# Kernel optimization log

Measured on AMD Instinct MI355X. Metric: run time of the kernel, lower is better.

Reference implementation:

```python
import jax, jax.numpy as jnp
import numpy as np

N_WORD, N_TOPIC, N_DOC = 50000, 2000, 50000
D_WORD, D_TOPIC, D_OUT = 256, 128, 128
E_WW, E_WT, E_WD, E_TD, E_TT = 500000, 400000, 500000, 400000, 300000


def setup_inputs() -> dict:
    key = jax.random.key(0)
    ks = jax.random.split(key, 32)
    i = iter(range(32))

    def randn(shape, scale=1.0):
        return jax.random.normal(ks[next(i)], shape, dtype=jnp.float32) * scale

    def edges(n_e, n_src, n_dst):
        src = jax.random.randint(ks[next(i)], (n_e,), 0, n_src, dtype=jnp.int32)
        dst = jax.random.randint(ks[next(i)], (n_e,), 0, n_dst, dtype=jnp.int32)
        w = jax.random.uniform(ks[next(i)], (n_e,), dtype=jnp.float32)
        return src, dst, w

    feat_word = randn((N_WORD, D_WORD))
    feat_topic = randn((N_TOPIC, D_TOPIC))
    ww_src, ww_dst, ww_w = edges(E_WW, N_WORD, N_WORD)
    wt_src, wt_dst, wt_w = edges(E_WT, N_WORD, N_TOPIC)
    wd_src, wd_dst, wd_w = edges(E_WD, N_WORD, N_DOC)
    td_src, td_dst, td_w = edges(E_TD, N_TOPIC, N_DOC)
    tt_src, tt_dst, tt_w = edges(E_TT, N_TOPIC, N_TOPIC)
    return dict(
        feat_word=feat_word, feat_topic=feat_topic,
        ww_src=ww_src, ww_dst=ww_dst, ww_w=ww_w,
        wt_src=wt_src, wt_dst=wt_dst, wt_w=wt_w,
        wd_src=wd_src, wd_dst=wd_dst, wd_w=wd_w,
        td_src=td_src, td_dst=td_dst, td_w=td_w,
        tt_src=tt_src, tt_dst=tt_dst, tt_w=tt_w,
        W_ww=randn((D_WORD, D_OUT), 0.02), b_ww=randn((D_OUT,), 0.02),
        W_wt=randn((D_WORD, D_OUT), 0.02), b_wt=randn((D_OUT,), 0.02),
        W_wd=randn((D_WORD, D_OUT), 0.02), b_wd=randn((D_OUT,), 0.02),
        W_td=randn((D_TOPIC, D_OUT), 0.02), b_td=randn((D_OUT,), 0.02),
        W_tt=randn((D_TOPIC, D_OUT), 0.02), b_tt=randn((D_OUT,), 0.02),
    )


def _mean_agg(Wh, src, dst, w, n_dst):
    # u_mul_e: gather src feature, scale by edge weight; fn.mean: divide by in-degree
    m = Wh[src] * w[:, None]                                   # [E, D_OUT]
    s = jax.ops.segment_sum(m, dst, num_segments=n_dst)        # [n_dst, D_OUT]
    deg = jax.ops.segment_sum(jnp.ones_like(w), dst, num_segments=n_dst)
    return jnp.where(deg[:, None] > 0, s / jnp.maximum(deg, 1.0)[:, None], 0.0)


def reference(feat_word, feat_topic,
              ww_src, ww_dst, ww_w, wt_src, wt_dst, wt_w,
              wd_src, wd_dst, wd_w, td_src, td_dst, td_w,
              tt_src, tt_dst, tt_w,
              W_ww, b_ww, W_wt, b_wt, W_wd, b_wd, W_td, b_td, W_tt, b_tt):
    # Per-relation projections (note: in the torch source the causal/noise
    # branches are overwritten by the plain Linear, so this is the effective math).
    Wh_ww = feat_word @ W_ww + b_ww
    Wh_wt = feat_word @ W_wt + b_wt
    Wh_wd = feat_word @ W_wd + b_wd
    Wh_td = feat_topic @ W_td + b_td
    Wh_tt = feat_topic @ W_tt + b_tt
    # mean per edge type, then cross-etype 'sum' per destination node type
    h_word = _mean_agg(Wh_ww, ww_src, ww_dst, ww_w, N_WORD)
    h_topic = (_mean_agg(Wh_wt, wt_src, wt_dst, wt_w, N_TOPIC)
               + _mean_agg(Wh_tt, tt_src, tt_dst, tt_w, N_TOPIC))
    h_doc = (_mean_agg(Wh_wd, wd_src, wd_dst, wd_w, N_DOC)
             + _mean_agg(Wh_td, td_src, td_dst, td_w, N_DOC))
    return h_word, h_topic, h_doc
```

## Files before the change

kernel.cpp:

```cpp
#include <hip/hip_runtime.h>

typedef short short8 __attribute__((ext_vector_type(8)));
typedef float floatx4 __attribute__((ext_vector_type(4)));

__device__ __forceinline__ float b2f(unsigned int u16) {
    union { unsigned int i; float f; } v;
    v.i = u16 << 16;
    return v.f;
}
__device__ __forceinline__ unsigned short f2b(float f) {
    unsigned int i = __float_as_uint(f);
    unsigned int r = (i + 0x7FFFu + ((i >> 16) & 1u)) >> 16;
    return (unsigned short)r;
}

#define N_WORD  50000
#define N_TOPIC 2000
#define N_DOC   50000
#define E_MAX   500000
#define CHAIN_END 0xFFFFFFFFu
#define NB_GEMM 814

__global__ void detect_kernel(const unsigned int* __restrict__ feat_u32,
                              unsigned int* __restrict__ flag)
{
    int cnt = 0;
    for (int i = 0; i < 256; ++i) {
        unsigned int u = feat_u32[i];
        int e = (u >> 7) & 0xFF;
        if (e >= 110 && e <= 140) ++cnt;
    }
    *flag = (cnt > 128) ? 1u : 0u;
}

__global__ __launch_bounds__(256) void swizzle_kernel(
    const void* __restrict__ W0, const void* __restrict__ W1,
    const void* __restrict__ W2, const void* __restrict__ W3,
    const void* __restrict__ W4,
    const void* __restrict__ b0, const void* __restrict__ b1,
    const void* __restrict__ b2, const void* __restrict__ b3,
    const void* __restrict__ b4,
    short8* __restrict__ D0, short8* __restrict__ D1,
    short8* __restrict__ D2, short8* __restrict__ D3,
    short8* __restrict__ D4,
    unsigned short* __restrict__ bias_out,
    const unsigned int* __restrict__ flag_p)
{
    const int w = blockIdx.y;
    const void* W; const void* bs; short8* D; int S;
    switch (w) {
        case 0: W = W0; bs = b0; D = D0; S = 8; break;
        case 1: W = W1; bs = b1; D = D1; S = 8; break;
        case 2: W = W2; bs = b2; D = D2; S = 8; break;
        case 3: W = W3; bs = b3; D = D3; S = 4; break;
        default: W = W4; bs = b4; D = D4; S = 4; break;
    }
    const int n_entries = S * 8 * 64;
    const int mode = (int)*flag_p;
    for (int e = blockIdx.x * 256 + threadIdx.x; e < n_entries; e += 8 * 256) {
        const int lane = e & 63, t = (e >> 6) & 7, s = e >> 9;
        const int q = lane >> 4, n = t * 16 + (lane & 15);
        short8 val;
#pragma unroll
        for (int j = 0; j < 8; ++j) {
            const int k = s * 32 + q * 8 + j;
            unsigned short hv = mode ? ((const unsigned short*)W)[k * 128 + n]
                                     : f2b(((const float*)W)[k * 128 + n]);
            val[j] = (short)hv;
        }
        D[e] = val;
    }
    if (blockIdx.x == 0 && threadIdx.x < 128) {
        bias_out[w * 128 + threadIdx.x] =
            mode ? ((const unsigned short*)bs)[threadIdx.x]
                 : f2b(((const float*)bs)[threadIdx.x]);
    }
}

template <int S, int NP>
__device__ __forceinline__ void gemm_body_lds(
    short8* __restrict__ Blds,
    const void* feat_, int n_rows, int bx,
    const short8* Ba, const short8* Bb, const short8* Bc,
    const unsigned short* bias_all, int ba, int bb, int bc,
    unsigned short* Oa, unsigned short* Ob, unsigned short* Oc,
    int mode_bf16)
{
    const int tid = threadIdx.x;
    const int lane = tid & 63;
    const int wave = tid >> 6;
    const int row0 = (bx * 4 + wave) * 16;
    const int m = lane & 15, q = lane >> 4;
    const int K = S * 32;
    int arow_idx = row0 + m;
    if (arow_idx >= n_rows) arow_idx = n_rows - 1;

    short8 a[S];
    if (mode_bf16) {
        const short8* arow = (const short8*)((const unsigned short*)feat_ + (size_t)arow_idx * K);
#pragma unroll
        for (int s = 0; s < S; ++s) a[s] = arow[s * 4 + q];
    } else {
        const float* arow = (const float*)feat_ + (size_t)arow_idx * K;
#pragma unroll
        for (int s = 0; s < S; ++s) {
            const float4 f0 = ((const float4*)arow)[s * 8 + q * 2];
            const float4 f1 = ((const float4*)arow)[s * 8 + q * 2 + 1];
            short8 t;
            t[0] = (short)f2b(f0.x); t[1] = (short)f2b(f0.y);
            t[2] = (short)f2b(f0.z); t[3] = (short)f2b(f0.w);
            t[4] = (short)f2b(f1.x); t[5] = (short)f2b(f1.y);
            t[6] = (short)f2b(f1.z); t[7] = (short)f2b(f1.w);
            a[s] = t;
        }
    }

    constexpr int NH = (S * 8 * 64 > 2048) ? 2 : 1;
    constexpr int SH = S / NH;

#pragma unroll
    for (int p = 0; p < NP; ++p) {
        const short8* B = (p == 0) ? Ba : ((p == 1) ? Bb : Bc);
        const unsigned short* bias = bias_all + ((p == 0) ? ba : ((p == 1) ? bb : bc)) * 128;
        unsigned short* O = (p == 0) ? Oa : ((p == 1) ? Ob : Oc);

        floatx4 acc[8];
#pragma unroll
        for (int t = 0; t < 8; ++t) { acc[t][0] = 0.f; acc[t][1] = 0.f; acc[t][2] = 0.f; acc[t][3] = 0.f; }

#pragma unroll
        for (int h = 0; h < NH; ++h) {
            __syncthreads();
            for (int i = tid; i < SH * 8 * 64; i += 256) Blds[i] = B[h * (SH * 8 * 64) + i];
            __syncthreads();
#pragma unroll
            for (int s = 0; s < SH; ++s) {
#pragma unroll
                for (int t = 0; t < 8; ++t) {
                    short8 b = Blds[(s * 8 + t) * 64 + lane];
                    acc[t] = __builtin_amdgcn_mfma_f32_16x16x32_bf16(a[h * SH + s], b, acc[t], 0, 0, 0);
                }
            }
        }

#pragma unroll
        for (int t = 0; t < 8; ++t) {
            const float bb_ = b2f((unsigned int)bias[t * 16 + m]);
#pragma unroll
            for (int r = 0; r < 4; ++r) {
                const int row = row0 + q * 4 + r;
                if (row < n_rows)
                    O[(size_t)row * 128 + t * 16 + m] = f2b(acc[t][r] + bb_);
            }
        }
    }
}

__global__ __launch_bounds__(256) void link_gemm_kernel(
    const void* __restrict__ feat_word, const void* __restrict__ feat_topic,
    const short8* __restrict__ Bww, const short8* __restrict__ Bwt,
    const short8* __restrict__ Bwd, const short8* __restrict__ Btt,
    const short8* __restrict__ Btd,
    const unsigned short* __restrict__ bias_all,
    unsigned short* __restrict__ Wh_ww, unsigned short* __restrict__ Wh_wt,
    unsigned short* __restrict__ Wh_wd, unsigned short* __restrict__ Wh_tt,
    unsigned short* __restrict__ Wh_td,
    const int* s0, const int* d0, const void* w0, int n0, unsigned int* h0, unsigned long long* e0,
    const int* s1, const int* d1, const void* w1, int n1, unsigned int* h1, unsigned long long* e1,
    const int* s2, const int* d2, const void* w2, int n2, unsigned int* h2, unsigned long long* e2,
    const int* s3, const int* d3, const void* w3, int n3, unsigned int* h3, unsigned long long* e3,
    const int* s4, const int* d4, const void* w4, int n4, unsigned int* h4, unsigned long long* e4,
    const unsigned int* __restrict__ flag_p)
{
    __shared__ short8 Blds[2048];
    const int mode = (int)*flag_p;

    if (blockIdx.x < NB_GEMM) {
        if (blockIdx.x < 782) {
            gemm_body_lds<8, 3>(Blds, feat_word, N_WORD, blockIdx.x, Bww, Bwt, Bwd,
                                bias_all, 0, 1, 2, Wh_ww, Wh_wt, Wh_wd, mode);
        } else {
            gemm_body_lds<4, 2>(Blds, feat_topic, N_TOPIC, blockIdx.x - 782, Btt, Btd,
                                (const short8*)nullptr, bias_all, 4, 3, 0,
                                Wh_tt, Wh_td, (unsigned short*)nullptr, mode);
        }
        return;
    }

    int lb = blockIdx.x - NB_GEMM;
    const int nb0 = (n0 + 255) >> 8, nb1 = (n1 + 255) >> 8, nb2 = (n2 + 255) >> 8,
              nb3 = (n3 + 255) >> 8;
    const int* src; const int* dst; const void* w_; int n;
    unsigned int* head; unsigned long long* ent; int H;
    if (lb < nb0)      { src = s0; dst = d0; w_ = w0; n = n0; head = h0; ent = e0; H = 1; }
    else if ((lb -= nb0) < nb1) { src = s1; dst = d1; w_ = w1; n = n1; head = h1; ent = e1; H = 4; }
    else if ((lb -= nb1) < nb2) { src = s2; dst = d2; w_ = w2; n = n2; head = h2; ent = e2; H = 4; }
    else if ((lb -= nb2) < nb3) { src = s3; dst = d3; w_ = w3; n = n3; head = h3; ent = e3; H = 1; }
    else { lb -= nb3;  src = s4; dst = d4; w_ = w4; n = n4; head = h4; ent = e4; H = 1; }

    const int i = lb * 256 + threadIdx.x;
    if (i >= n) return;
    const int d = dst[i];
    const unsigned int slot = (unsigned int)d * H + ((unsigned int)i & (H - 1));
    const unsigned int old = atomicExch(&head[slot], (unsigned int)i);
    const unsigned short w16 = mode ? ((const unsigned short*)w_)[i]
                                    : f2b(((const float*)w_)[i]);
    ent[i] = ((unsigned long long)old << 32)
           | ((unsigned long long)w16 << 16)
           | (unsigned long long)(unsigned int)src[i];
}

__device__ __forceinline__ void chain8(
    const unsigned long long* __restrict__ ent,
    const unsigned short* __restrict__ Wh,
    unsigned int e, int sl, float a[8], float& cnt)
{
    while (e != CHAIN_END) {
        const unsigned long long v = ent[e];
        const unsigned int lo = (unsigned int)v;
        e = (unsigned int)(v >> 32);
        const float w = b2f(lo >> 16);
        const uint4 u = ((const uint4*)(Wh + (size_t)(lo & 0xffffu) * 128))[sl];
        a[0] += b2f(u.x & 0xffffu) * w; a[1] += b2f(u.x >> 16) * w;
        a[2] += b2f(u.y & 0xffffu) * w; a[3] += b2f(u.y >> 16) * w;
        a[4] += b2f(u.z & 0xffffu) * w; a[5] += b2f(u.z >> 16) * w;
        a[6] += b2f(u.w & 0xffffu) * w; a[7] += b2f(u.w >> 16) * w;
        cnt += 1.0f;
    }
}

__device__ __forceinline__ void write8(
    void* out, size_t off_elems, int node, int sl, const float r[8], int mode)
{
    if (mode) {
        uint4 o;
        o.x = (unsigned int)f2b(r[0]) | ((unsigned int)f2b(r[1]) << 16);
        o.y = (unsigned int)f2b(r[2]) | ((unsigned int)f2b(r[3]) << 16);
        o.z = (unsigned int)f2b(r[4]) | ((unsigned int)f2b(r[5]) << 16);
        o.w = (unsigned int)f2b(r[6]) | ((unsigned int)f2b(r[7]) << 16);
        *(uint4*)((unsigned short*)out + off_elems + (size_t)node * 128 + sl * 8) = o;
    } else {
        float* p = (float*)out + off_elems + (size_t)node * 128 + sl * 8;
        ((float4*)p)[0] = make_float4(r[0], r[1], r[2], r[3]);
        ((float4*)p)[1] = make_float4(r[4], r[5], r[6], r[7]);
    }
}

__global__ __launch_bounds__(256) void gather_dt_kernel(
    const unsigned int* __restrict__ h_wt, const unsigned long long* __restrict__ e_wt,
    const unsigned short* __restrict__ Wh_wt,
    const unsigned int* __restrict__ h_tt, const unsigned long long* __restrict__ e_tt,
    const unsigned short* __restrict__ Wh_tt,
    const unsigned int* __restrict__ h_wd, const unsigned long long* __restrict__ e_wd,
    const unsigned short* __restrict__ Wh_wd,
    const unsigned int* __restrict__ h_td, const unsigned long long* __restrict__ e_td,
    const unsigned short* __restrict__ Wh_td,
    void* __restrict__ out,
    const unsigned int* __restrict__ flag_p)
{
    const int mode = (int)*flag_p;
    const int sl = threadIdx.x & 15;

    if (blockIdx.x < 500) {
        const int wave = threadIdx.x >> 6;
        const int grp  = (threadIdx.x >> 4) & 3;
        const int node = blockIdx.x * 4 + wave;
        float r[8] = {0, 0, 0, 0, 0, 0, 0, 0};
        {
            float a[8] = {0, 0, 0, 0, 0, 0, 0, 0}; float cnt = 0.f;
            chain8(e_wt, Wh_wt, h_wt[node * 4 + grp], sl, a, cnt);
#pragma unroll
            for (int j = 0; j < 8; ++j) { a[j] += __shfl_xor(a[j], 16); a[j] += __shfl_xor(a[j], 32); }
            cnt += __shfl_xor(cnt, 16); cnt += __shfl_xor(cnt, 32);
            const float inv = (cnt > 0.f) ? 1.f / cnt : 0.f;
#pragma unroll
            for (int j = 0; j < 8; ++j) r[j] += a[j] * inv;
        }
        {
            float a[8] = {0, 0, 0, 0, 0, 0, 0, 0}; float cnt = 0.f;
            chain8(e_tt, Wh_tt, h_tt[node * 4 + grp], sl, a, cnt);
#pragma unroll
            for (int j = 0; j < 8; ++j) { a[j] += __shfl_xor(a[j], 16); a[j] += __shfl_xor(a[j], 32); }
            cnt += __shfl_xor(cnt, 16); cnt += __shfl_xor(cnt, 32);
            const float inv = (cnt > 0.f) ? 1.f / cnt : 0.f;
#pragma unroll
            for (int j = 0; j < 8; ++j) r[j] += a[j] * inv;
        }
        if (grp == 0) write8(out, (size_t)6400000, node, sl, r, mode);
    } else {
        const int sub = threadIdx.x >> 4;
        const int node = (blockIdx.x - 500) * 16 + sub;
        float r[8] = {0, 0, 0, 0, 0, 0, 0, 0};
        {
            float a[8] = {0, 0, 0, 0, 0, 0, 0, 0}; float cnt = 0.f;
            chain8(e_wd, Wh_wd, h_wd[node], sl, a, cnt);
            const float inv = (cnt > 0.f) ? 1.f / cnt : 0.f;
#pragma unroll
            for (int j = 0; j < 8; ++j) r[j] += a[j] * inv;
        }
        {
            float a[8] = {0, 0, 0, 0, 0, 0, 0, 0}; float cnt = 0.f;
            chain8(e_td, Wh_td, h_td[node], sl, a, cnt);
            const float inv = (cnt > 0.f) ? 1.f / cnt : 0.f;
#pragma unroll
            for (int j = 0; j < 8; ++j) r[j] += a[j] * inv;
        }
        write8(out, (size_t)6656000, node, sl, r, mode);
    }
}

__global__ __launch_bounds__(256) void gather_w_kernel(
    const unsigned int* __restrict__ h_ww, const unsigned long long* __restrict__ e_ww,
    const unsigned short* __restrict__ Wh_ww,
    void* __restrict__ out,
    const unsigned int* __restrict__ flag_p)
{
    const int mode = (int)*flag_p;
    const int sl = threadIdx.x & 15;
    const int sub = threadIdx.x >> 4;
    const int node = blockIdx.x * 16 + sub;
    float a[8] = {0, 0, 0, 0, 0, 0, 0, 0}; float cnt = 0.f;
    chain8(e_ww, Wh_ww, h_ww[node], sl, a, cnt);
    const float inv = (cnt > 0.f) ? 1.f / cnt : 0.f;
#pragma unroll
    for (int j = 0; j < 8; ++j) a[j] *= inv;
    write8(out, 0, node, sl, a, mode);
}

extern "C" void kernel_launch(void* const* d_in, const int* in_sizes, int n_in,
                              void* d_out, int out_size, void* d_ws, size_t ws_size,
                              hipStream_t stream)
{
    const void* feat_word  = d_in[0];
    const void* feat_topic = d_in[1];
    const int* ww_src = (const int*)d_in[2];
    const int* ww_dst = (const int*)d_in[3];
    const void* ww_w = d_in[4];
    const int* wt_src = (const int*)d_in[5];
    const int* wt_dst = (const int*)d_in[6];
    const void* wt_w = d_in[7];
    const int* wd_src = (const int*)d_in[8];
    const int* wd_dst = (const int*)d_in[9];
    const void* wd_w = d_in[10];
    const int* td_src = (const int*)d_in[11];
    const int* td_dst = (const int*)d_in[12];
    const void* td_w = d_in[13];
    const int* tt_src = (const int*)d_in[14];
    const int* tt_dst = (const int*)d_in[15];
    const void* tt_w = d_in[16];
    const void* W_ww = d_in[17];
    const void* b_ww = d_in[18];
    const void* W_wt = d_in[19];
    const void* b_wt = d_in[20];
    const void* W_wd = d_in[21];
    const void* b_wd = d_in[22];
    const void* W_td = d_in[23];
    const void* b_td = d_in[24];
    const void* W_tt = d_in[25];
    const void* b_tt = d_in[26];

    const int E_ww = in_sizes[2];
    const int E_wt = in_sizes[5];
    const int E_wd = in_sizes[8];
    const int E_td = in_sizes[11];
    const int E_tt = in_sizes[14];

    char* ws = (char*)d_ws;
    unsigned int* flag = (unsigned int*)ws;
    unsigned int* head_base = (unsigned int*)(ws + 4);
    unsigned int* h_ww = head_base;
    unsigned int* h_wt = h_ww + 50000;
    unsigned int* h_tt = h_wt + 8000;
    unsigned int* h_wd = h_tt + 8000;
    unsigned int* h_td = h_wd + 50000;
    size_t off = 4 + (size_t)166000 * 4;
    off = (off + 15) & ~(size_t)15;
    short8* Bsw_ww = (short8*)(ws + off); off += 65536;
    short8* Bsw_wt = (short8*)(ws + off); off += 65536;
    short8* Bsw_wd = (short8*)(ws + off); off += 65536;
    short8* Bsw_td = (short8*)(ws + off); off += 32768;
    short8* Bsw_tt = (short8*)(ws + off); off += 32768;
    unsigned short* bias_all = (unsigned short*)(ws + off); off += 5 * 128 * 2;
    off = (off + 15) & ~(size_t)15;
    unsigned short* Wh_ww = (unsigned short*)(ws + off); off += (size_t)N_WORD * 128 * 2;
    unsigned short* Wh_wt = (unsigned short*)(ws + off); off += (size_t)N_WORD * 128 * 2;
    unsigned short* Wh_tt = (unsigned short*)(ws + off); off += (size_t)N_TOPIC * 128 * 2;
    unsigned short* Wh_td = (unsigned short*)(ws + off); off += (size_t)N_TOPIC * 128 * 2;
    off = (off + 7) & ~(size_t)7;
    unsigned long long* e_ww = (unsigned long long*)(ws + off); off += (size_t)E_MAX * 8;
    unsigned long long* e_wt = (unsigned long long*)(ws + off); off += (size_t)E_MAX * 8;
    unsigned long long* e_tt = (unsigned long long*)(ws + off); off += (size_t)E_MAX * 8;
    unsigned long long* e_wd = (unsigned long long*)(ws + off); off += (size_t)E_MAX * 8;
    unsigned long long* e_td = (unsigned long long*)(ws + off); off += (size_t)E_MAX * 8;

    unsigned short* Wh_wd = (unsigned short*)d_out;

    detect_kernel<<<1, 1, 0, stream>>>((const unsigned int*)feat_word, flag);
    hipMemsetAsync(head_base, 0xFF, (size_t)166000 * 4, stream);

    swizzle_kernel<<<dim3(8, 5), 256, 0, stream>>>(
        W_ww, W_wt, W_wd, W_td, W_tt, b_ww, b_wt, b_wd, b_td, b_tt,
        Bsw_ww, Bsw_wt, Bsw_wd, Bsw_td, Bsw_tt, bias_all, flag);

    const int nb_link = ((E_ww + 255) / 256) + ((E_wt + 255) / 256) +
                        ((E_tt + 255) / 256) + ((E_wd + 255) / 256) +
                        ((E_td + 255) / 256);
    link_gemm_kernel<<<NB_GEMM + nb_link, 256, 0, stream>>>(
        feat_word, feat_topic, Bsw_ww, Bsw_wt, Bsw_wd, Bsw_tt, Bsw_td,
        bias_all, Wh_ww, Wh_wt, Wh_wd, Wh_tt, Wh_td,
        ww_src, ww_dst, ww_w, E_ww, h_ww, e_ww,
        wt_src, wt_dst, wt_w, E_wt, h_wt, e_wt,
        tt_src, tt_dst, tt_w, E_tt, h_tt, e_tt,
        wd_src, wd_dst, wd_w, E_wd, h_wd, e_wd,
        td_src, td_dst, td_w, E_td, h_td, e_td, flag);

    gather_dt_kernel<<<500 + 3125, 256, 0, stream>>>(
        h_wt, e_wt, Wh_wt, h_tt, e_tt, Wh_tt,
        h_wd, e_wd, Wh_wd, h_td, e_td, Wh_td, d_out, flag);

    gather_w_kernel<<<3125, 256, 0, stream>>>(
        h_ww, e_ww, Wh_ww, d_out, flag);
}
```

Measured before the change: 402.4 us.

## Interleave GEMM and link blocks, batch edge linking, fuse gather kernels

Link blocks now process four edges per thread, and GEMM blocks are interleaved with link blocks (2 of every 7) so the two kinds of work overlap on the device instead of running in sequence. When the workspace is large enough, Wh_wd moves from the output buffer into the workspace. That removes the ordering hazard with the word gather, so the topic, doc and word gathers run in a single fused kernel launch instead of two. The cost is extra workspace and more index arithmetic, and the added atomics per thread may raise contention.

```diff
diff --git a/kernel.cpp b/kernel.cpp
--- a/kernel.cpp
+++ b/kernel.cpp
@@ -174,22 +174,29 @@
 {
     __shared__ short8 Blds[2048];
     const int mode = (int)*flag_p;
-
-    if (blockIdx.x < NB_GEMM) {
-        if (blockIdx.x < 782) {
-            gemm_body_lds<8, 3>(Blds, feat_word, N_WORD, blockIdx.x, Bww, Bwt, Bwd,
-                                bias_all, 0, 1, 2, Wh_ww, Wh_wt, Wh_wd, mode);
-        } else {
-            gemm_body_lds<4, 2>(Blds, feat_topic, N_TOPIC, blockIdx.x - 782, Btt, Btd,
-                                (const short8*)nullptr, bias_all, 4, 3, 0,
-                                Wh_tt, Wh_td, (unsigned short*)nullptr, mode);
+    const int bid = blockIdx.x;
+    const int q7 = bid / 7, r7 = bid % 7;
+
+    if (r7 < 2) {
+        const int gid = q7 * 2 + r7;
+        if (gid < NB_GEMM) {
+            if (gid < 782) {
+                gemm_body_lds<8, 3>(Blds, feat_word, N_WORD, gid, Bww, Bwt, Bwd,
+                                    bias_all, 0, 1, 2, Wh_ww, Wh_wt, Wh_wd, mode);
+            } else {
+                gemm_body_lds<4, 2>(Blds, feat_topic, N_TOPIC, gid - 782, Btt, Btd,
+                                    (const short8*)nullptr, bias_all, 4, 3, 0,
+                                    Wh_tt, Wh_td, (unsigned short*)nullptr, mode);
+            }
+            return;
         }
-        return;
-    }
-
-    int lb = blockIdx.x - NB_GEMM;
-    const int nb0 = (n0 + 255) >> 8, nb1 = (n1 + 255) >> 8, nb2 = (n2 + 255) >> 8,
-              nb3 = (n3 + 255) >> 8;
+    }
+
+    const int cnt_g = min(q7 * 2 + min(r7, 2), NB_GEMM);
+    int lb = bid - cnt_g;
+
+    const int nb0 = (n0 + 1023) >> 10, nb1 = (n1 + 1023) >> 10,
+              nb2 = (n2 + 1023) >> 10, nb3 = (n3 + 1023) >> 10;
     const int* src; const int* dst; const void* w_; int n;
     unsigned int* head; unsigned long long* ent; int H;
     if (lb < nb0)      { src = s0; dst = d0; w_ = w0; n = n0; head = h0; ent = e0; H = 1; }
@@ -198,16 +205,27 @@
     else if ((lb -= nb2) < nb3) { src = s3; dst = d3; w_ = w3; n = n3; head = h3; ent = e3; H = 1; }
     else { lb -= nb3;  src = s4; dst = d4; w_ = w4; n = n4; head = h4; ent = e4; H = 1; }
 
-    const int i = lb * 256 + threadIdx.x;
-    if (i >= n) return;
-    const int d = dst[i];
-    const unsigned int slot = (unsigned int)d * H + ((unsigned int)i & (H - 1));
-    const unsigned int old = atomicExch(&head[slot], (unsigned int)i);
-    const unsigned short w16 = mode ? ((const unsigned short*)w_)[i]
-                                    : f2b(((const float*)w_)[i]);
-    ent[i] = ((unsigned long long)old << 32)
-           | ((unsigned long long)w16 << 16)
-           | (unsigned long long)(unsigned int)src[i];
+    const int i0 = lb * 1024 + threadIdx.x;
+    bool val[4]; int iv[4]; unsigned long long lo[4]; unsigned int oldv[4];
+#pragma unroll
+    for (int u = 0; u < 4; ++u) {
+        const int i = i0 + u * 256;
+        iv[u] = i;
+        val[u] = (i < n);
+        if (val[u]) {
+            const int d = dst[i];
+            const unsigned short w16 = mode ? ((const unsigned short*)w_)[i]
+                                            : f2b(((const float*)w_)[i]);
+            lo[u] = ((unsigned long long)w16 << 16)
+                  | (unsigned long long)(unsigned int)src[i];
+            const unsigned int slot = (unsigned int)d * H + ((unsigned int)i & (H - 1));
+            oldv[u] = atomicExch(&head[slot], (unsigned int)i);
+        }
+    }
+#pragma unroll
+    for (int u = 0; u < 4; ++u)
+        if (val[u])
+            ent[iv[u]] = ((unsigned long long)oldv[u] << 32) | lo[u];
 }
 
 __device__ __forceinline__ void chain8(
@@ -246,6 +264,110 @@
     }
 }
 
+__device__ __forceinline__ void topic_body(
+    const unsigned int* __restrict__ h_wt, const unsigned long long* __restrict__ e_wt,
+    const unsigned short* __restrict__ Wh_wt,
+    const unsigned int* __restrict__ h_tt, const unsigned long long* __restrict__ e_tt,
+    const unsigned short* __restrict__ Wh_tt,
+    void* __restrict__ out, int blk, int mode)
+{
+    const int sl = threadIdx.x & 15;
+    const int wave = threadIdx.x >> 6;
+    const int grp  = (threadIdx.x >> 4) & 3;
+    const int node = blk * 4 + wave;
+    float r[8] = {0, 0, 0, 0, 0, 0, 0, 0};
+    {
+        float a[8] = {0, 0, 0, 0, 0, 0, 0, 0}; float cnt = 0.f;
+        chain8(e_wt, Wh_wt, h_wt[node * 4 + grp], sl, a, cnt);
+#pragma unroll
+        for (int j = 0; j < 8; ++j) { a[j] += __shfl_xor(a[j], 16); a[j] += __shfl_xor(a[j], 32); }
+        cnt += __shfl_xor(cnt, 16); cnt += __shfl_xor(cnt, 32);
+        const float inv = (cnt > 0.f) ? 1.f / cnt : 0.f;
+#pragma unroll
+        for (int j = 0; j < 8; ++j) r[j] += a[j] * inv;
+    }
+    {
+        float a[8] = {0, 0, 0, 0, 0, 0, 0, 0}; float cnt = 0.f;
+        chain8(e_tt, Wh_tt, h_tt[node * 4 + grp], sl, a, cnt);
+#pragma unroll
+        for (int j = 0; j < 8; ++j) { a[j] += __shfl_xor(a[j], 16); a[j] += __shfl_xor(a[j], 32); }
+        cnt += __shfl_xor(cnt, 16); cnt += __shfl_xor(cnt, 32);
+        const float inv = (cnt > 0.f) ? 1.f / cnt : 0.f;
+#pragma unroll
+        for (int j = 0; j < 8; ++j) r[j] += a[j] * inv;
+    }
+    if (grp == 0) write8(out, (size_t)6400000, node, sl, r, mode);
+}
+
+__device__ __forceinline__ void doc_body(
+    const unsigned int* __restrict__ h_a, const unsigned long long* __restrict__ e_a,
+    const unsigned short* __restrict__ Wh_a,
+    const unsigned int* __restrict__ h_b, const unsigned long long* __restrict__ e_b,
+    const unsigned short* __restrict__ Wh_b,
+    void* __restrict__ out, size_t off_elems, int blk, int mode)
+{
+    const int sl = threadIdx.x & 15;
+    const int sub = threadIdx.x >> 4;
+    const int node = blk * 16 + sub;
+    float r[8] = {0, 0, 0, 0, 0, 0, 0, 0};
+    {
+        float a[8] = {0, 0, 0, 0, 0, 0, 0, 0}; float cnt = 0.f;
+        chain8(e_a, Wh_a, h_a[node], sl, a, cnt);
+        const float inv = (cnt > 0.f) ? 1.f / cnt : 0.f;
+#pragma unroll
+        for (int j = 0; j < 8; ++j) r[j] += a[j] * inv;
+    }
+    {
+        float a[8] = {0, 0, 0, 0, 0, 0, 0, 0}; float cnt = 0.f;
+        chain8(e_b, Wh_b, h_b[node], sl, a, cnt);
+        const float inv = (cnt > 0.f) ? 1.f / cnt : 0.f;
+#pragma unroll
+        for (int j = 0; j < 8; ++j) r[j] += a[j] * inv;
+    }
+    write8(out, off_elems, node, sl, r, mode);
+}
+
+__device__ __forceinline__ void word_body(
+    const unsigned int* __restrict__ h_ww, const unsigned long long* __restrict__ e_ww,
+    const unsigned short* __restrict__ Wh_ww,
+    void* __restrict__ out, int blk, int mode)
+{
+    const int sl = threadIdx.x & 15;
+    const int sub = threadIdx.x >> 4;
+    const int node = blk * 16 + sub;
+    float a[8] = {0, 0, 0, 0, 0, 0, 0, 0}; float cnt = 0.f;
+    chain8(e_ww, Wh_ww, h_ww[node], sl, a, cnt);
+    const float inv = (cnt > 0.f) ? 1.f / cnt : 0.f;
+#pragma unroll
+    for (int j = 0; j < 8; ++j) a[j] *= inv;
+    write8(out, 0, node, sl, a, mode);
+}
+
+__global__ __launch_bounds__(256) void gather_all_kernel(
+    const unsigned int* __restrict__ h_wt, const unsigned long long* __restrict__ e_wt,
+    const unsigned short* __restrict__ Wh_wt,
+    const unsigned int* __restrict__ h_tt, const unsigned long long* __restrict__ e_tt,
+    const unsigned short* __restrict__ Wh_tt,
+    const unsigned int* __restrict__ h_wd, const unsigned long long* __restrict__ e_wd,
+    const unsigned short* __restrict__ Wh_wd,
+    const unsigned int* __restrict__ h_td, const unsigned long long* __restrict__ e_td,
+    const unsigned short* __restrict__ Wh_td,
+    const unsigned int* __restrict__ h_ww, const unsigned long long* __restrict__ e_ww,
+    const unsigned short* __restrict__ Wh_ww,
+    void* __restrict__ out,
+    const unsigned int* __restrict__ flag_p)
+{
+    const int mode = (int)*flag_p;
+    if (blockIdx.x < 500) {
+        topic_body(h_wt, e_wt, Wh_wt, h_tt, e_tt, Wh_tt, out, blockIdx.x, mode);
+    } else if (blockIdx.x < 3625) {
+        doc_body(h_wd, e_wd, Wh_wd, h_td, e_td, Wh_td,
+                 out, (size_t)6656000, blockIdx.x - 500, mode);
+    } else {
+        word_body(h_ww, e_ww, Wh_ww, out, blockIdx.x - 3625, mode);
+    }
+}
+
 __global__ __launch_bounds__(256) void gather_dt_kernel(
     const unsigned int* __restrict__ h_wt, const unsigned long long* __restrict__ e_wt,
     const unsigned short* __restrict__ Wh_wt,
@@ -259,53 +381,11 @@
     const unsigned int* __restrict__ flag_p)
 {
     const int mode = (int)*flag_p;
-    const int sl = threadIdx.x & 15;
-
     if (blockIdx.x < 500) {
-        const int wave = threadIdx.x >> 6;
-        const int grp  = (threadIdx.x >> 4) & 3;
-        const int node = blockIdx.x * 4 + wave;
-        float r[8] = {0, 0, 0, 0, 0, 0, 0, 0};
-        {
-            float a[8] = {0, 0, 0, 0, 0, 0, 0, 0}; float cnt = 0.f;
-            chain8(e_wt, Wh_wt, h_wt[node * 4 + grp], sl, a, cnt);
-#pragma unroll
-            for (int j = 0; j < 8; ++j) { a[j] += __shfl_xor(a[j], 16); a[j] += __shfl_xor(a[j], 32); }
-            cnt += __shfl_xor(cnt, 16); cnt += __shfl_xor(cnt, 32);
-            const float inv = (cnt > 0.f) ? 1.f / cnt : 0.f;
-#pragma unroll
-            for (int j = 0; j < 8; ++j) r[j] += a[j] * inv;
-        }
-        {
-            float a[8] = {0, 0, 0, 0, 0, 0, 0, 0}; float cnt = 0.f;
-            chain8(e_tt, Wh_tt, h_tt[node * 4 + grp], sl, a, cnt);
-#pragma unroll
-            for (int j = 0; j < 8; ++j) { a[j] += __shfl_xor(a[j], 16); a[j] += __shfl_xor(a[j], 32); }
-            cnt += __shfl_xor(cnt, 16); cnt += __shfl_xor(cnt, 32);
-            const float inv = (cnt > 0.f) ? 1.f / cnt : 0.f;
-#pragma unroll
-            for (int j = 0; j < 8; ++j) r[j] += a[j] * inv;
-        }
-        if (grp == 0) write8(out, (size_t)6400000, node, sl, r, mode);
+        topic_body(h_wt, e_wt, Wh_wt, h_tt, e_tt, Wh_tt, out, blockIdx.x, mode);
     } else {
-        const int sub = threadIdx.x >> 4;
-        const int node = (blockIdx.x - 500) * 16 + sub;
-        float r[8] = {0, 0, 0, 0, 0, 0, 0, 0};
-        {
-            float a[8] = {0, 0, 0, 0, 0, 0, 0, 0}; float cnt = 0.f;
-            chain8(e_wd, Wh_wd, h_wd[node], sl, a, cnt);
-            const float inv = (cnt > 0.f) ? 1.f / cnt : 0.f;
-#pragma unroll
-            for (int j = 0; j < 8; ++j) r[j] += a[j] * inv;
-        }
-        {
-            float a[8] = {0, 0, 0, 0, 0, 0, 0, 0}; float cnt = 0.f;
-            chain8(e_td, Wh_td, h_td[node], sl, a, cnt);
-            const float inv = (cnt > 0.f) ? 1.f / cnt : 0.f;
-#pragma unroll
-            for (int j = 0; j < 8; ++j) r[j] += a[j] * inv;
-        }
-        write8(out, (size_t)6656000, node, sl, r, mode);
+        doc_body(h_wd, e_wd, Wh_wd, h_td, e_td, Wh_td,
+                 out, (size_t)6656000, blockIdx.x - 500, mode);
     }
 }
 
@@ -315,16 +395,7 @@
     void* __restrict__ out,
     const unsigned int* __restrict__ flag_p)
 {
-    const int mode = (int)*flag_p;
-    const int sl = threadIdx.x & 15;
-    const int sub = threadIdx.x >> 4;
-    const int node = blockIdx.x * 16 + sub;
-    float a[8] = {0, 0, 0, 0, 0, 0, 0, 0}; float cnt = 0.f;
-    chain8(e_ww, Wh_ww, h_ww[node], sl, a, cnt);
-    const float inv = (cnt > 0.f) ? 1.f / cnt : 0.f;
-#pragma unroll
-    for (int j = 0; j < 8; ++j) a[j] *= inv;
-    write8(out, 0, node, sl, a, mode);
+    word_body(h_ww, e_ww, Wh_ww, out, blockIdx.x, (int)*flag_p);
 }
 
 extern "C" void kernel_launch(void* const* d_in, const int* in_sizes, int n_in,
@@ -393,7 +464,11 @@
     unsigned long long* e_wd = (unsigned long long*)(ws + off); off += (size_t)E_MAX * 8;
     unsigned long long* e_td = (unsigned long long*)(ws + off); off += (size_t)E_MAX * 8;
 
-    unsigned short* Wh_wd = (unsigned short*)d_out;
+    off = (off + 15) & ~(size_t)15;
+    const size_t whwd_bytes = (size_t)N_WORD * 128 * 2;
+    const bool fuse_gather = (ws_size >= off + whwd_bytes);
+    unsigned short* Wh_wd = fuse_gather ? (unsigned short*)(ws + off)
+                                        : (unsigned short*)d_out;
 
     detect_kernel<<<1, 1, 0, stream>>>((const unsigned int*)feat_word, flag);
     hipMemsetAsync(head_base, 0xFF, (size_t)166000 * 4, stream);
@@ -402,10 +477,12 @@
         W_ww, W_wt, W_wd, W_td, W_tt, b_ww, b_wt, b_wd, b_td, b_tt,
         Bsw_ww, Bsw_wt, Bsw_wd, Bsw_td, Bsw_tt, bias_all, flag);
 
-    const int nb_link = ((E_ww + 255) / 256) + ((E_wt + 255) / 256) +
-                        ((E_tt + 255) / 256) + ((E_wd + 255) / 256) +
-                        ((E_td + 255) / 256);
-    link_gemm_kernel<<<NB_GEMM + nb_link, 256, 0, stream>>>(
+    const int nb_link = ((E_ww + 1023) / 1024) + ((E_wt + 1023) / 1024) +
+                        ((E_tt + 1023) / 1024) + ((E_wd + 1023) / 1024) +
+                        ((E_td + 1023) / 1024);
+    int n_blocks = NB_GEMM + nb_link;
+    if (n_blocks < 2844) n_blocks = 2844;
+    link_gemm_kernel<<<n_blocks, 256, 0, stream>>>(
         feat_word, feat_topic, Bsw_ww, Bsw_wt, Bsw_wd, Bsw_tt, Bsw_td,
         bias_all, Wh_ww, Wh_wt, Wh_wd, Wh_tt, Wh_td,
         ww_src, ww_dst, ww_w, E_ww, h_ww, e_ww,
@@ -414,10 +491,16 @@
         wd_src, wd_dst, wd_w, E_wd, h_wd, e_wd,
         td_src, td_dst, td_w, E_td, h_td, e_td, flag);
 
-    gather_dt_kernel<<<500 + 3125, 256, 0, stream>>>(
-        h_wt, e_wt, Wh_wt, h_tt, e_tt, Wh_tt,
-        h_wd, e_wd, Wh_wd, h_td, e_td, Wh_td, d_out, flag);
-
-    gather_w_kernel<<<3125, 256, 0, stream>>>(
-        h_ww, e_ww, Wh_ww, d_out, flag);
-}
+    if (fuse_gather) {
+        gather_all_kernel<<<500 + 3125 + 3125, 256, 0, stream>>>(
+            h_wt, e_wt, Wh_wt, h_tt, e_tt, Wh_tt,
+            h_wd, e_wd, Wh_wd, h_td, e_td, Wh_td,
+            h_ww, e_ww, Wh_ww, d_out, flag);
+    } else {
+        gather_dt_kernel<<<500 + 3125, 256, 0, stream>>>(
+            h_wt, e_wt, Wh_wt, h_tt, e_tt, Wh_tt,
+            h_wd, e_wd, Wh_wd, h_td, e_td, Wh_td, d_out, flag);
+        gather_w_kernel<<<3125, 256, 0, stream>>>(
+            h_ww, e_ww, Wh_ww, d_out, flag);
+    }
+}
```

Measured after the change: 401.6 us. Within noise of the previous version (-0.2%).

## Split all edge chains four ways, prefetch chain links, and fuse gathers into one kernel

Applied to the files above, without the earlier changes.

Every relation's linked-list head now uses four sub-chains per destination node. Each node is handled by a full wave that reduces the sub-chains with shuffles, which shortens serial pointer-chasing depth. The chain walk prefetches the next entry while gathering the current row, and walks two relations at once to overlap their latencies. When workspace allows, Wh_wd is moved out of the output buffer so all three gathers fuse into one launch. In exchange, head-array memset size grows and the gather launches use four times as many blocks, with more shuffle-reduction work.

```diff
diff --git a/kernel.cpp b/kernel.cpp
--- a/kernel.cpp
+++ b/kernel.cpp
@@ -20,6 +20,12 @@
 #define E_MAX   500000
 #define CHAIN_END 0xFFFFFFFFu
 #define NB_GEMM 814
+#define NSLOT_WW 200000
+#define NSLOT_WT 8000
+#define NSLOT_TT 8000
+#define NSLOT_WD 200000
+#define NSLOT_TD 200000
+#define NSLOT_ALL (NSLOT_WW + NSLOT_WT + NSLOT_TT + NSLOT_WD + NSLOT_TD)
 
 __global__ void detect_kernel(const unsigned int* __restrict__ feat_u32,
                               unsigned int* __restrict__ flag)
@@ -191,17 +197,17 @@
     const int nb0 = (n0 + 255) >> 8, nb1 = (n1 + 255) >> 8, nb2 = (n2 + 255) >> 8,
               nb3 = (n3 + 255) >> 8;
     const int* src; const int* dst; const void* w_; int n;
-    unsigned int* head; unsigned long long* ent; int H;
-    if (lb < nb0)      { src = s0; dst = d0; w_ = w0; n = n0; head = h0; ent = e0; H = 1; }
-    else if ((lb -= nb0) < nb1) { src = s1; dst = d1; w_ = w1; n = n1; head = h1; ent = e1; H = 4; }
-    else if ((lb -= nb1) < nb2) { src = s2; dst = d2; w_ = w2; n = n2; head = h2; ent = e2; H = 4; }
-    else if ((lb -= nb2) < nb3) { src = s3; dst = d3; w_ = w3; n = n3; head = h3; ent = e3; H = 1; }
-    else { lb -= nb3;  src = s4; dst = d4; w_ = w4; n = n4; head = h4; ent = e4; H = 1; }
+    unsigned int* head; unsigned long long* ent;
+    if (lb < nb0)      { src = s0; dst = d0; w_ = w0; n = n0; head = h0; ent = e0; }
+    else if ((lb -= nb0) < nb1) { src = s1; dst = d1; w_ = w1; n = n1; head = h1; ent = e1; }
+    else if ((lb -= nb1) < nb2) { src = s2; dst = d2; w_ = w2; n = n2; head = h2; ent = e2; }
+    else if ((lb -= nb2) < nb3) { src = s3; dst = d3; w_ = w3; n = n3; head = h3; ent = e3; }
+    else { lb -= nb3;  src = s4; dst = d4; w_ = w4; n = n4; head = h4; ent = e4; }
 
     const int i = lb * 256 + threadIdx.x;
     if (i >= n) return;
     const int d = dst[i];
-    const unsigned int slot = (unsigned int)d * H + ((unsigned int)i & (H - 1));
+    const unsigned int slot = (unsigned int)d * 4 + ((unsigned int)i & 3);
     const unsigned int old = atomicExch(&head[slot], (unsigned int)i);
     const unsigned short w16 = mode ? ((const unsigned short*)w_)[i]
                                     : f2b(((const float*)w_)[i]);
@@ -210,22 +216,52 @@
            | (unsigned long long)(unsigned int)src[i];
 }
 
-__device__ __forceinline__ void chain8(
+__device__ __forceinline__ void acc8(float a[8], const uint4& u, float w)
+{
+    a[0] += b2f(u.x & 0xffffu) * w; a[1] += b2f(u.x >> 16) * w;
+    a[2] += b2f(u.y & 0xffffu) * w; a[3] += b2f(u.y >> 16) * w;
+    a[4] += b2f(u.z & 0xffffu) * w; a[5] += b2f(u.z >> 16) * w;
+    a[6] += b2f(u.w & 0xffffu) * w; a[7] += b2f(u.w >> 16) * w;
+}
+
+__device__ __forceinline__ void walk1(
     const unsigned long long* __restrict__ ent,
     const unsigned short* __restrict__ Wh,
     unsigned int e, int sl, float a[8], float& cnt)
 {
-    while (e != CHAIN_END) {
-        const unsigned long long v = ent[e];
-        const unsigned int lo = (unsigned int)v;
-        e = (unsigned int)(v >> 32);
-        const float w = b2f(lo >> 16);
-        const uint4 u = ((const uint4*)(Wh + (size_t)(lo & 0xffffu) * 128))[sl];
-        a[0] += b2f(u.x & 0xffffu) * w; a[1] += b2f(u.x >> 16) * w;
-        a[2] += b2f(u.y & 0xffffu) * w; a[3] += b2f(u.y >> 16) * w;
-        a[4] += b2f(u.z & 0xffffu) * w; a[5] += b2f(u.z >> 16) * w;
-        a[6] += b2f(u.w & 0xffffu) * w; a[7] += b2f(u.w >> 16) * w;
+    bool live = (e != CHAIN_END);
+    unsigned long long v = ent[live ? e : 0];
+    while (live) {
+        const unsigned int nx = (unsigned int)(v >> 32);
+        const bool live_n = (nx != CHAIN_END);
+        const unsigned long long vn = ent[live_n ? nx : 0];
+        const uint4 u = ((const uint4*)(Wh + (size_t)((unsigned int)v & 0xffffu) * 128))[sl];
+        acc8(a, u, b2f(((unsigned int)v) >> 16));
         cnt += 1.0f;
+        v = vn; live = live_n;
+    }
+}
+
+__device__ __forceinline__ void walk2(
+    const unsigned long long* __restrict__ ent1, const unsigned short* __restrict__ Wh1, unsigned int e1,
+    const unsigned long long* __restrict__ ent2, const unsigned short* __restrict__ Wh2, unsigned int e2,
+    int sl, float a1[8], float a2[8], float& c1, float& c2)
+{
+    bool l1 = (e1 != CHAIN_END), l2 = (e2 != CHAIN_END);
+    unsigned long long v1 = ent1[l1 ? e1 : 0];
+    unsigned long long v2 = ent2[l2 ? e2 : 0];
+    while (l1 || l2) {
+        const unsigned int n1 = (unsigned int)(v1 >> 32);
+        const unsigned int n2 = (unsigned int)(v2 >> 32);
+        const bool l1n = l1 && (n1 != CHAIN_END);
+        const bool l2n = l2 && (n2 != CHAIN_END);
+        const unsigned long long v1n = ent1[l1n ? n1 : 0];
+        const unsigned long long v2n = ent2[l2n ? n2 : 0];
+        const uint4 u1 = ((const uint4*)(Wh1 + (size_t)((unsigned int)v1 & 0xffffu) * 128))[sl];
+        const uint4 u2 = ((const uint4*)(Wh2 + (size_t)((unsigned int)v2 & 0xffffu) * 128))[sl];
+        if (l1) { acc8(a1, u1, b2f(((unsigned int)v1) >> 16)); c1 += 1.0f; }
+        if (l2) { acc8(a2, u2, b2f(((unsigned int)v2) >> 16)); c2 += 1.0f; }
+        v1 = v1n; v2 = v2n; l1 = l1n; l2 = l2n;
     }
 }
 
@@ -246,6 +282,83 @@
     }
 }
 
+__device__ __forceinline__ void dual_body(
+    const unsigned int* __restrict__ h1, const unsigned long long* __restrict__ e1t,
+    const unsigned short* __restrict__ Wh1,
+    const unsigned int* __restrict__ h2, const unsigned long long* __restrict__ e2t,
+    const unsigned short* __restrict__ Wh2,
+    void* __restrict__ out, size_t off_elems, int blk, int mode)
+{
+    const int sl = threadIdx.x & 15;
+    const int grp = (threadIdx.x >> 4) & 3;
+    const int wave = threadIdx.x >> 6;
+    const int node = blk * 4 + wave;
+    float a1[8] = {0,0,0,0,0,0,0,0}, a2[8] = {0,0,0,0,0,0,0,0};
+    float c1 = 0.f, c2 = 0.f;
+    walk2(e1t, Wh1, h1[node * 4 + grp], e2t, Wh2, h2[node * 4 + grp],
+          sl, a1, a2, c1, c2);
+#pragma unroll
+    for (int j = 0; j < 8; ++j) {
+        a1[j] += __shfl_xor(a1[j], 16); a1[j] += __shfl_xor(a1[j], 32);
+        a2[j] += __shfl_xor(a2[j], 16); a2[j] += __shfl_xor(a2[j], 32);
+    }
+    c1 += __shfl_xor(c1, 16); c1 += __shfl_xor(c1, 32);
+    c2 += __shfl_xor(c2, 16); c2 += __shfl_xor(c2, 32);
+    const float i1 = (c1 > 0.f) ? 1.f / c1 : 0.f;
+    const float i2 = (c2 > 0.f) ? 1.f / c2 : 0.f;
+    float r[8];
+#pragma unroll
+    for (int j = 0; j < 8; ++j) r[j] = a1[j] * i1 + a2[j] * i2;
+    if (grp == 0) write8(out, off_elems, node, sl, r, mode);
+}
+
+__device__ __forceinline__ void word_body(
+    const unsigned int* __restrict__ h_ww, const unsigned long long* __restrict__ e_ww,
+    const unsigned short* __restrict__ Wh_ww,
+    void* __restrict__ out, int blk, int mode)
+{
+    const int sl = threadIdx.x & 15;
+    const int grp = (threadIdx.x >> 4) & 3;
+    const int wave = threadIdx.x >> 6;
+    const int node = blk * 4 + wave;
+    float a[8] = {0,0,0,0,0,0,0,0}; float cnt = 0.f;
+    walk1(e_ww, Wh_ww, h_ww[node * 4 + grp], sl, a, cnt);
+#pragma unroll
+    for (int j = 0; j < 8; ++j) { a[j] += __shfl_xor(a[j], 16); a[j] += __shfl_xor(a[j], 32); }
+    cnt += __shfl_xor(cnt, 16); cnt += __shfl_xor(cnt, 32);
+    const float inv = (cnt > 0.f) ? 1.f / cnt : 0.f;
+    float r[8];
+#pragma unroll
+    for (int j = 0; j < 8; ++j) r[j] = a[j] * inv;
+    if (grp == 0) write8(out, 0, node, sl, r, mode);
+}
+
+__global__ __launch_bounds__(256) void gather_all_kernel(
+    const unsigned int* __restrict__ h_wt, const unsigned long long* __restrict__ e_wt,
+    const unsigned short* __restrict__ Wh_wt,
+    const unsigned int* __restrict__ h_tt, const unsigned long long* __restrict__ e_tt,
+    const unsigned short* __restrict__ Wh_tt,
+    const unsigned int* __restrict__ h_wd, const unsigned long long* __restrict__ e_wd,
+    const unsigned short* __restrict__ Wh_wd,
+    const unsigned int* __restrict__ h_td, const unsigned long long* __restrict__ e_td,
+    const unsigned short* __restrict__ Wh_td,
+    const unsigned int* __restrict__ h_ww, const unsigned long long* __restrict__ e_ww,
+    const unsigned short* __restrict__ Wh_ww,
+    void* __restrict__ out,
+    const unsigned int* __restrict__ flag_p)
+{
+    const int mode = (int)*flag_p;
+    if (blockIdx.x < 500) {
+        dual_body(h_wt, e_wt, Wh_wt, h_tt, e_tt, Wh_tt,
+                  out, (size_t)6400000, blockIdx.x, mode);
+    } else if (blockIdx.x < 13000) {
+        dual_body(h_wd, e_wd, Wh_wd, h_td, e_td, Wh_td,
+                  out, (size_t)6656000, blockIdx.x - 500, mode);
+    } else {
+        word_body(h_ww, e_ww, Wh_ww, out, blockIdx.x - 13000, mode);
+    }
+}
+
 __global__ __launch_bounds__(256) void gather_dt_kernel(
     const unsigned int* __restrict__ h_wt, const unsigned long long* __restrict__ e_wt,
     const unsigned short* __restrict__ Wh_wt,
@@ -259,53 +372,12 @@
     const unsigned int* __restrict__ flag_p)
 {
     const int mode = (int)*flag_p;
-    const int sl = threadIdx.x & 15;
-
     if (blockIdx.x < 500) {
-        const int wave = threadIdx.x >> 6;
-        const int grp  = (threadIdx.x >> 4) & 3;
-        const int node = blockIdx.x * 4 + wave;
-        float r[8] = {0, 0, 0, 0, 0, 0, 0, 0};
-        {
-            float a[8] = {0, 0, 0, 0, 0, 0, 0, 0}; float cnt = 0.f;
-            chain8(e_wt, Wh_wt, h_wt[node * 4 + grp], sl, a, cnt);
-#pragma unroll
-            for (int j = 0; j < 8; ++j) { a[j] += __shfl_xor(a[j], 16); a[j] += __shfl_xor(a[j], 32); }
-            cnt += __shfl_xor(cnt, 16); cnt += __shfl_xor(cnt, 32);
-            const float inv = (cnt > 0.f) ? 1.f / cnt : 0.f;
-#pragma unroll
-            for (int j = 0; j < 8; ++j) r[j] += a[j] * inv;
-        }
-        {
-            float a[8] = {0, 0, 0, 0, 0, 0, 0, 0}; float cnt = 0.f;
-            chain8(e_tt, Wh_tt, h_tt[node * 4 + grp], sl, a, cnt);
-#pragma unroll
-            for (int j = 0; j < 8; ++j) { a[j] += __shfl_xor(a[j], 16); a[j] += __shfl_xor(a[j], 32); }
-            cnt += __shfl_xor(cnt, 16); cnt += __shfl_xor(cnt, 32);
-            const float inv = (cnt > 0.f) ? 1.f / cnt : 0.f;
-#pragma unroll
-            for (int j = 0; j < 8; ++j) r[j] += a[j] * inv;
-        }
-        if (grp == 0) write8(out, (size_t)6400000, node, sl, r, mode);
+        dual_body(h_wt, e_wt, Wh_wt, h_tt, e_tt, Wh_tt,
+                  out, (size_t)6400000, blockIdx.x, mode);
     } else {
-        const int sub = threadIdx.x >> 4;
-        const int node = (blockIdx.x - 500) * 16 + sub;
-        float r[8] = {0, 0, 0, 0, 0, 0, 0, 0};
-        {
-            float a[8] = {0, 0, 0, 0, 0, 0, 0, 0}; float cnt = 0.f;
-            chain8(e_wd, Wh_wd, h_wd[node], sl, a, cnt);
-            const float inv = (cnt > 0.f) ? 1.f / cnt : 0.f;
-#pragma unroll
-            for (int j = 0; j < 8; ++j) r[j] += a[j] * inv;
-        }
-        {
-            float a[8] = {0, 0, 0, 0, 0, 0, 0, 0}; float cnt = 0.f;
-            chain8(e_td, Wh_td, h_td[node], sl, a, cnt);
-            const float inv = (cnt > 0.f) ? 1.f / cnt : 0.f;
-#pragma unroll
-            for (int j = 0; j < 8; ++j) r[j] += a[j] * inv;
-        }
-        write8(out, (size_t)6656000, node, sl, r, mode);
+        dual_body(h_wd, e_wd, Wh_wd, h_td, e_td, Wh_td,
+                  out, (size_t)6656000, blockIdx.x - 500, mode);
     }
 }
 
@@ -315,16 +387,7 @@
     void* __restrict__ out,
     const unsigned int* __restrict__ flag_p)
 {
-    const int mode = (int)*flag_p;
-    const int sl = threadIdx.x & 15;
-    const int sub = threadIdx.x >> 4;
-    const int node = blockIdx.x * 16 + sub;
-    float a[8] = {0, 0, 0, 0, 0, 0, 0, 0}; float cnt = 0.f;
-    chain8(e_ww, Wh_ww, h_ww[node], sl, a, cnt);
-    const float inv = (cnt > 0.f) ? 1.f / cnt : 0.f;
-#pragma unroll
-    for (int j = 0; j < 8; ++j) a[j] *= inv;
-    write8(out, 0, node, sl, a, mode);
+    word_body(h_ww, e_ww, Wh_ww, out, blockIdx.x, (int)*flag_p);
 }
 
 extern "C" void kernel_launch(void* const* d_in, const int* in_sizes, int n_in,
@@ -369,11 +432,11 @@
     unsigned int* flag = (unsigned int*)ws;
     unsigned int* head_base = (unsigned int*)(ws + 4);
     unsigned int* h_ww = head_base;
-    unsigned int* h_wt = h_ww + 50000;
-    unsigned int* h_tt = h_wt + 8000;
-    unsigned int* h_wd = h_tt + 8000;
-    unsigned int* h_td = h_wd + 50000;
-    size_t off = 4 + (size_t)166000 * 4;
+    unsigned int* h_wt = h_ww + NSLOT_WW;
+    unsigned int* h_tt = h_wt + NSLOT_WT;
+    unsigned int* h_wd = h_tt + NSLOT_TT;
+    unsigned int* h_td = h_wd + NSLOT_WD;
+    size_t off = 4 + (size_t)NSLOT_ALL * 4;
     off = (off + 15) & ~(size_t)15;
     short8* Bsw_ww = (short8*)(ws + off); off += 65536;
     short8* Bsw_wt = (short8*)(ws + off); off += 65536;
@@ -393,10 +456,14 @@
     unsigned long long* e_wd = (unsigned long long*)(ws + off); off += (size_t)E_MAX * 8;
     unsigned long long* e_td = (unsigned long long*)(ws + off); off += (size_t)E_MAX * 8;
 
-    unsigned short* Wh_wd = (unsigned short*)d_out;
+    off = (off + 15) & ~(size_t)15;
+    const size_t whwd_bytes = (size_t)N_WORD * 128 * 2;
+    const bool fuse_gather = (ws_size >= off + whwd_bytes);
+    unsigned short* Wh_wd = fuse_gather ? (unsigned short*)(ws + off)
+                                        : (unsigned short*)d_out;
 
     detect_kernel<<<1, 1, 0, stream>>>((const unsigned int*)feat_word, flag);
-    hipMemsetAsync(head_base, 0xFF, (size_t)166000 * 4, stream);
+    hipMemsetAsync(head_base, 0xFF, (size_t)NSLOT_ALL * 4, stream);
 
     swizzle_kernel<<<dim3(8, 5), 256, 0, stream>>>(
         W_ww, W_wt, W_wd, W_td, W_tt, b_ww, b_wt, b_wd, b_td, b_tt,
@@ -414,10 +481,16 @@
         wd_src, wd_dst, wd_w, E_wd, h_wd, e_wd,
         td_src, td_dst, td_w, E_td, h_td, e_td, flag);
 
-    gather_dt_kernel<<<500 + 3125, 256, 0, stream>>>(
-        h_wt, e_wt, Wh_wt, h_tt, e_tt, Wh_tt,
-        h_wd, e_wd, Wh_wd, h_td, e_td, Wh_td, d_out, flag);
-
-    gather_w_kernel<<<3125, 256, 0, stream>>>(
-        h_ww, e_ww, Wh_ww, d_out, flag);
-}
+    if (fuse_gather) {
+        gather_all_kernel<<<500 + 12500 + 12500, 256, 0, stream>>>(
+            h_wt, e_wt, Wh_wt, h_tt, e_tt, Wh_tt,
+            h_wd, e_wd, Wh_wd, h_td, e_td, Wh_td,
+            h_ww, e_ww, Wh_ww, d_out, flag);
+    } else {
+        gather_dt_kernel<<<500 + 12500, 256, 0, stream>>>(
+            h_wt, e_wt, Wh_wt, h_tt, e_tt, Wh_tt,
+            h_wd, e_wd, Wh_wd, h_td, e_td, Wh_td, d_out, flag);
+        gather_w_kernel<<<12500, 256, 0, stream>>>(
+            h_ww, e_ww, Wh_ww, d_out, flag);
+    }
+}
```

Result: faster. 381.1 us (-5.3%).
